# Kernel optimization log

Hardware: AMD Instinct MI355X
Metric: run time of the kernel (lower is better)

Reference implementation:

```python
import jax, jax.numpy as jnp
import numpy as np

N_NODES = 50000
N_EDGES = 800000
HIDDEN = 128
DIST_BUCKETS = 20


def setup_inputs() -> dict:
    key = jax.random.key(0)
    k = jax.random.split(key, 6)
    x = jax.random.normal(k[0], (N_NODES, HIDDEN), dtype=jnp.float32)
    edge_index = jax.random.randint(k[1], (2, N_EDGES), 0, N_NODES, dtype=jnp.int64)
    distances = jax.random.randint(k[2], (N_EDGES,), 0, 999, dtype=jnp.int64)
    W1 = jax.random.normal(k[3], (2 * HIDDEN, HIDDEN), dtype=jnp.float32) * 0.1
    W2 = jax.random.normal(k[4], (2 * HIDDEN, 1), dtype=jnp.float32) * 0.1
    dist_emb_table = jax.random.normal(k[5], (DIST_BUCKETS, HIDDEN), dtype=jnp.float32) * 0.1
    return {"x": x, "edge_index": edge_index, "distances": distances,
            "W1": W1, "W2": W2, "dist_emb_table": dist_emb_table}


def reference(x, edge_index, distances, W1, W2, dist_emb_table):
    n_nodes = x.shape[0]
    buckets = distances // 50                          # [E] in [0, 20)
    src = x[edge_index[0]]                             # [E, H]
    tgt = x[edge_index[1]]                             # [E, H]
    h = jnp.concatenate([src, tgt], axis=1) @ W1       # [E, H]
    h = jax.nn.leaky_relu(h, negative_slope=0.2)
    de = dist_emb_table[buckets]                       # [E, H]
    att = jnp.concatenate([h, de], axis=1) @ W2        # [E, 1]
    att = jnp.exp(jax.nn.sigmoid(att))                 # [E, 1]
    src_w = src * att                                  # [E, H]
    agg = jax.ops.segment_sum(src_w, edge_index[1], num_segments=n_nodes)   # [N, H]
    att_agg = jax.ops.segment_sum(att, edge_index[1], num_segments=n_nodes) # [N, 1]
    out = agg / (att_agg + 1e-6)
    return jax.nn.relu(out)
```

## Files before the change

### kernel.cpp

```cpp
#include <hip/hip_runtime.h>

#define HIDDEN 128
#define NBUCKETS 20
#define CSRCAP 64

typedef unsigned int uint32;
typedef unsigned short u16;
typedef unsigned long long u64;
typedef __attribute__((ext_vector_type(8))) short bf16x8;
typedef __attribute__((ext_vector_type(4))) float f32x4;

__device__ __forceinline__ u16 f32_to_bf16(float f) {
    uint32 u = __float_as_uint(f);
    return (u16)((u + 0x7fffu + ((u >> 16) & 1u)) >> 16);
}
__device__ __forceinline__ float bf_lo(uint32 u) { return __uint_as_float(u << 16); }
__device__ __forceinline__ float bf_hi(uint32 u) { return __uint_as_float(u & 0xffff0000u); }

__global__ void prep_kernel(const float* __restrict__ W1, u16* __restrict__ W1T,
                            int* __restrict__ cur, int n_nodes,
                            const float* __restrict__ table,
                            const float* __restrict__ W2,
                            float* __restrict__ de_dot) {
    int idx = blockIdx.x * 256 + threadIdx.x;
    int n = idx >> 7, k = idx & 127;
    int srow = (n < 128) ? k : (128 + k);
    W1T[idx] = f32_to_bf16(W1[srow * HIDDEN + (n & 127)]);
    for (int i = idx; i < n_nodes; i += 32768) cur[i] = 0;
    if (blockIdx.x < 5) {
        int w = blockIdx.x * 4 + (threadIdx.x >> 6);
        int lane = threadIdx.x & 63;
        if (w < NBUCKETS) {
            float a = fmaf(table[w * HIDDEN + lane], W2[HIDDEN + lane],
                           table[w * HIDDEN + 64 + lane] * W2[HIDDEN + 64 + lane]);
#pragma unroll
            for (int off = 32; off > 0; off >>= 1) a += __shfl_xor(a, off, 64);
            if (lane == 0) de_dot[w] = a;
        }
    }
}

__global__ __launch_bounds__(256)
void gemm_scatter_kernel(const float* __restrict__ x, const u16* __restrict__ W1T,
                         const int* __restrict__ edge_index,
                         const int* __restrict__ distances,
                         int* __restrict__ cur, uint32* __restrict__ csr_sb,
                         uint32* __restrict__ xyu, u16* __restrict__ z16,
                         int n_nodes, int n_edges) {
    __shared__ bf16x8 lds_a[16][16];
    __shared__ u16 lds_c[4][16][72];

    int tid = threadIdx.x;

    int e = blockIdx.x * 256 + tid;
    if (e < n_edges) {
        int s = edge_index[e];
        int t = edge_index[n_edges + e];
        uint32 bk = (uint32)(distances[e] / 50);
        int pos = atomicAdd(&cur[t], 1);
        csr_sb[((size_t)t << 6) + pos] = (uint32)s | (bk << 16);
    }

    int row_base = blockIdx.x * 16;
    if (row_base >= n_nodes) return;

    {
        int row = tid >> 4, c = tid & 15;
        int node = row_base + row;
        bf16x8 a = {};
        if (node < n_nodes) {
            const float4* xp = (const float4*)(x + (size_t)node * HIDDEN + c * 8);
            float4 v0 = xp[0], v1 = xp[1];
            a[0] = (short)f32_to_bf16(v0.x); a[1] = (short)f32_to_bf16(v0.y);
            a[2] = (short)f32_to_bf16(v0.z); a[3] = (short)f32_to_bf16(v0.w);
            a[4] = (short)f32_to_bf16(v1.x); a[5] = (short)f32_to_bf16(v1.y);
            a[6] = (short)f32_to_bf16(v1.z); a[7] = (short)f32_to_bf16(v1.w);
        }
        lds_a[c][row] = a;
    }
    __syncthreads();

    int wave = tid >> 6, lane = tid & 63;
    int m = lane & 15, kb = lane >> 4;

    bf16x8 afrag[4];
#pragma unroll
    for (int ks = 0; ks < 4; ++ks) afrag[ks] = lds_a[ks * 4 + kb][m];

#pragma unroll
    for (int ci = 0; ci < 4; ++ci) {
        int col = wave * 64 + ci * 16 + m;
        const u16* bp = W1T + (size_t)col * HIDDEN + kb * 8;
        f32x4 acc = {0.f, 0.f, 0.f, 0.f};
#pragma unroll
        for (int ks = 0; ks < 4; ++ks) {
            bf16x8 b = *(const bf16x8*)(bp + ks * 32);
            acc = __builtin_amdgcn_mfma_f32_16x16x32_bf16(afrag[ks], b, acc, 0, 0, 0);
        }
#pragma unroll
        for (int e2 = 0; e2 < 4; ++e2)
            lds_c[wave][kb * 4 + e2][ci * 16 + m] = f32_to_bf16(acc[e2]);
    }
    __syncthreads();

    {
        int r = lane >> 2, q = lane & 3;
        const u16* src = &lds_c[wave][r][q * 16];
        bf16x8 c0 = *(const bf16x8*)(src);
        bf16x8 c1 = *(const bf16x8*)(src + 8);
        int node = row_base + r;
        int colg = wave * 64 + q * 16;
        if (node < n_nodes) {
            if (colg < HIDDEN) {
                int ch = colg >> 3;
                bf16x8 xa = lds_a[ch][r];
                bf16x8 xb = lds_a[ch + 1][r];
                const uint32* xu0 = (const uint32*)&xa;
                const uint32* xu1 = (const uint32*)&xb;
                const uint32* yu0 = (const uint32*)&c0;
                const uint32* yu1 = (const uint32*)&c1;
                uint32 ow[16];
#pragma unroll
                for (int i = 0; i < 4; ++i) { ow[2*i]   = xu0[i]; ow[2*i+1]   = yu0[i]; }
#pragma unroll
                for (int i = 0; i < 4; ++i) { ow[8+2*i] = xu1[i]; ow[8+2*i+1] = yu1[i]; }
                uint32* dst = xyu + (size_t)node * 128 + colg;
#pragma unroll
                for (int i = 0; i < 4; ++i)
                    *(f32x4*)(dst + i * 4) = *(const f32x4*)(ow + i * 4);
            } else {
                u16* dst = z16 + (size_t)node * HIDDEN + colg - HIDDEN;
                *(bf16x8*)dst = c0;
                *(bf16x8*)(dst + 8) = c1;
            }
        }
    }
}

__global__ void aggregate_kernel(const uint32* __restrict__ xyu,
                                 const u16* __restrict__ z16,
                                 const float* __restrict__ W2,
                                 const uint32* __restrict__ csr_sb,
                                 const int* __restrict__ cur,
                                 const float* __restrict__ de_dot,
                                 float* __restrict__ out,
                                 int n_nodes) {
    __shared__ float d_lds[NBUCKETS];
    int tid = threadIdx.x;
    if (tid < NBUCKETS) d_lds[tid] = de_dot[tid];
    __syncthreads();

    int lane = tid & 63;
    int t = blockIdx.x * (blockDim.x >> 6) + (tid >> 6);
    if (t >= n_nodes) return;

    size_t base = (size_t)t << 6;
    int deg = cur[t];
    const uint2* __restrict__ xyp = (const uint2*)xyu;

    uint32 zv = ((const uint32*)z16)[(size_t)t * 64 + lane];
    float z0 = bf_lo(zv), z1 = bf_hi(zv);
    float2 wv = *(const float2*)(W2 + lane * 2);

    float acc0 = 0.f, acc1 = 0.f, attsum = 0.f;
    bool hiHalf = lane >= 32;
    bool hiQuarter = (lane & 16) != 0;

    for (int b = 0; b < deg; b += 64) {
        int nb = min(64, deg - b);
        uint32 rec_l = 0;
        float ded_l = 0.f;
        if (lane < nb) {
            rec_l = csr_sb[base + b + lane];
            ded_l = d_lds[rec_l >> 16];
        }
        int j = 0;
        for (; j + 4 <= nb; j += 4) {
            int sA = (int)(__shfl(rec_l, j, 64) & 0xFFFFu);
            int sB = (int)(__shfl(rec_l, j + 1, 64) & 0xFFFFu);
            int sC = (int)(__shfl(rec_l, j + 2, 64) & 0xFFFFu);
            int sD = (int)(__shfl(rec_l, j + 3, 64) & 0xFFFFu);
            float dA = __shfl(ded_l, j, 64);
            float dB = __shfl(ded_l, j + 1, 64);
            float dC = __shfl(ded_l, j + 2, 64);
            float dD = __shfl(ded_l, j + 3, 64);
            uint2 va = xyp[(size_t)sA * 64 + lane];
            uint2 vb = xyp[(size_t)sB * 64 + lane];
            uint2 vc = xyp[(size_t)sC * 64 + lane];
            uint2 vd = xyp[(size_t)sD * 64 + lane];
            float h;
            h = bf_lo(va.y) + z0; h = fmaxf(h, 0.2f * h); float pA = h * wv.x;
            h = bf_hi(va.y) + z1; h = fmaxf(h, 0.2f * h); pA = fmaf(h, wv.y, pA);
            h = bf_lo(vb.y) + z0; h = fmaxf(h, 0.2f * h); float pB = h * wv.x;
            h = bf_hi(vb.y) + z1; h = fmaxf(h, 0.2f * h); pB = fmaf(h, wv.y, pB);
            h = bf_lo(vc.y) + z0; h = fmaxf(h, 0.2f * h); float pC = h * wv.x;
            h = bf_hi(vc.y) + z1; h = fmaxf(h, 0.2f * h); pC = fmaf(h, wv.y, pC);
            h = bf_lo(vd.y) + z0; h = fmaxf(h, 0.2f * h); float pD = h * wv.x;
            h = bf_hi(vd.y) + z1; h = fmaxf(h, 0.2f * h); pD = fmaf(h, wv.y, pD);
            pA += __shfl_xor(pA, 32, 64);
            pB += __shfl_xor(pB, 32, 64);
            pC += __shfl_xor(pC, 32, 64);
            pD += __shfl_xor(pD, 32, 64);
            float rAB = hiHalf ? pB : pA;
            float rCD = hiHalf ? pD : pC;
            rAB += __shfl_xor(rAB, 16, 64);
            rCD += __shfl_xor(rCD, 16, 64);
            float rr = hiQuarter ? rCD : rAB;
#pragma unroll
            for (int off = 8; off > 0; off >>= 1) rr += __shfl_xor(rr, off, 64);
            float ded_e = hiQuarter ? (hiHalf ? dD : dC) : (hiHalf ? dB : dA);
            float att = __expf(1.f / (1.f + __expf(-(rr + ded_e))));
            float attA = __shfl(att, 0, 64);
            float attC = __shfl(att, 16, 64);
            float attB = __shfl(att, 32, 64);
            float attD = __shfl(att, 48, 64);
            acc0 = fmaf(attA, bf_lo(va.x), acc0);
            acc1 = fmaf(attA, bf_hi(va.x), acc1);
            acc0 = fmaf(attB, bf_lo(vb.x), acc0);
            acc1 = fmaf(attB, bf_hi(vb.x), acc1);
            acc0 = fmaf(attC, bf_lo(vc.x), acc0);
            acc1 = fmaf(attC, bf_hi(vc.x), acc1);
            acc0 = fmaf(attD, bf_lo(vd.x), acc0);
            acc1 = fmaf(attD, bf_hi(vd.x), acc1);
            attsum += (attA + attB) + (attC + attD);
        }
        for (; j < nb; ++j) {
            int sA = (int)(__shfl(rec_l, j, 64) & 0xFFFFu);
            float dA = __shfl(ded_l, j, 64);
            uint2 va = xyp[(size_t)sA * 64 + lane];
            float hA0 = bf_lo(va.y) + z0, hA1 = bf_hi(va.y) + z1;
            hA0 = fmaxf(hA0, 0.2f * hA0); hA1 = fmaxf(hA1, 0.2f * hA1);
            float pA = fmaf(hA0, wv.x, hA1 * wv.y);
#pragma unroll
            for (int off = 32; off > 0; off >>= 1) pA += __shfl_xor(pA, off, 64);
            float attA = __expf(1.f / (1.f + __expf(-(pA + dA))));
            acc0 = fmaf(attA, bf_lo(va.x), acc0);
            acc1 = fmaf(attA, bf_hi(va.x), acc1);
            attsum += attA;
        }
    }
    float inv = 1.f / (attsum + 1e-6f);
    float2 o;
    o.x = fmaxf(acc0 * inv, 0.f);
    o.y = fmaxf(acc1 * inv, 0.f);
    *(float2*)(out + (size_t)t * HIDDEN + lane * 2) = o;
}

static inline size_t align16(size_t v) { return (v + 15) & ~(size_t)15; }

extern "C" void kernel_launch(void* const* d_in, const int* in_sizes, int n_in,
                              void* d_out, int out_size, void* d_ws, size_t ws_size,
                              hipStream_t stream) {
    const float* x          = (const float*)d_in[0];
    const int*   edge_index = (const int*)d_in[1];
    const int*   distances  = (const int*)d_in[2];
    const float* W1         = (const float*)d_in[3];
    const float* W2         = (const float*)d_in[4];
    const float* table      = (const float*)d_in[5];

    int n_nodes = in_sizes[0] / HIDDEN;
    int n_edges = in_sizes[1] / 2;
    float* out = (float*)d_out;

    char* p = (char*)d_ws;
    int* cur       = (int*)p;                p += align16((size_t)n_nodes * 4);
    uint32* csr_sb = (uint32*)p;             p += align16((size_t)n_nodes * CSRCAP * 4);
    float* de_dot  = (float*)p;              p += align16(32 * 4);
    u16* W1T       = (u16*)p;                p += align16(256 * HIDDEN * 2);
    u16* z16       = (u16*)p;                p += align16((size_t)n_nodes * HIDDEN * 2);
    uint32* xyu    = (uint32*)p;

    prep_kernel<<<128, 256, 0, stream>>>(W1, W1T, cur, n_nodes, table, W2, de_dot);

    int ntiles = (n_nodes + 15) / 16;
    int eblocks = (n_edges + 255) / 256;
    int gblocks = (ntiles > eblocks) ? ntiles : eblocks;
    gemm_scatter_kernel<<<gblocks, 256, 0, stream>>>(
        x, W1T, edge_index, distances, cur, csr_sb, xyu, z16, n_nodes, n_edges);

    const int waves_per_block = 4;
    int ablocks = (n_nodes + waves_per_block - 1) / waves_per_block;
    aggregate_kernel<<<ablocks, 64 * waves_per_block, 0, stream>>>(
        xyu, z16, W2, csr_sb, cur, de_dot, out, n_nodes);
}
```

Measured before the change: 137.2 us.

## Process two edges and two GEMM row tiles per block, deferring atomics

Each block of the fused GEMM/scatter kernel now handles two edges per thread and two 16-row node tiles, halving the grid. Edge index and distance loads are issued up front, and the atomic CSR insertion is moved after the GEMM so the load latency overlaps with the matrix work. This amortizes per-block setup and W1T fragment loads across two tiles, at the cost of extra LDS, registers and an additional barrier per tile.

```diff
diff --git a/kernel.cpp b/kernel.cpp
--- a/kernel.cpp
+++ b/kernel.cpp
@@ -47,93 +47,118 @@
                          int* __restrict__ cur, uint32* __restrict__ csr_sb,
                          uint32* __restrict__ xyu, u16* __restrict__ z16,
                          int n_nodes, int n_edges) {
-    __shared__ bf16x8 lds_a[16][16];
+    __shared__ bf16x8 lds_a[2][16][16];
     __shared__ u16 lds_c[4][16][72];
 
     int tid = threadIdx.x;
 
-    int e = blockIdx.x * 256 + tid;
-    if (e < n_edges) {
-        int s = edge_index[e];
-        int t = edge_index[n_edges + e];
-        uint32 bk = (uint32)(distances[e] / 50);
-        int pos = atomicAdd(&cur[t], 1);
-        csr_sb[((size_t)t << 6) + pos] = (uint32)s | (bk << 16);
-    }
-
-    int row_base = blockIdx.x * 16;
-    if (row_base >= n_nodes) return;
-
-    {
-        int row = tid >> 4, c = tid & 15;
-        int node = row_base + row;
-        bf16x8 a = {};
-        if (node < n_nodes) {
-            const float4* xp = (const float4*)(x + (size_t)node * HIDDEN + c * 8);
-            float4 v0 = xp[0], v1 = xp[1];
-            a[0] = (short)f32_to_bf16(v0.x); a[1] = (short)f32_to_bf16(v0.y);
-            a[2] = (short)f32_to_bf16(v0.z); a[3] = (short)f32_to_bf16(v0.w);
-            a[4] = (short)f32_to_bf16(v1.x); a[5] = (short)f32_to_bf16(v1.y);
-            a[6] = (short)f32_to_bf16(v1.z); a[7] = (short)f32_to_bf16(v1.w);
-        }
-        lds_a[c][row] = a;
+    int e0 = blockIdx.x * 512 + tid;
+    int e1 = e0 + 256;
+    bool he0 = (e0 < n_edges), he1 = (e1 < n_edges);
+    int es0 = 0, et0 = 0, es1 = 0, et1 = 0;
+    uint32 bk0 = 0, bk1 = 0;
+    if (he0) {
+        es0 = edge_index[e0];
+        et0 = edge_index[n_edges + e0];
+        bk0 = (uint32)(distances[e0] / 50);
+    }
+    if (he1) {
+        es1 = edge_index[e1];
+        et1 = edge_index[n_edges + e1];
+        bk1 = (uint32)(distances[e1] / 50);
+    }
+
+    int rb0 = blockIdx.x * 32;
+
+#pragma unroll
+    for (int tt = 0; tt < 2; ++tt) {
+        int rb = rb0 + tt * 16;
+        if (rb < n_nodes) {
+            int row = tid >> 4, c = tid & 15;
+            int node = rb + row;
+            bf16x8 a = {};
+            if (node < n_nodes) {
+                const float4* xp = (const float4*)(x + (size_t)node * HIDDEN + c * 8);
+                float4 v0 = xp[0], v1 = xp[1];
+                a[0] = (short)f32_to_bf16(v0.x); a[1] = (short)f32_to_bf16(v0.y);
+                a[2] = (short)f32_to_bf16(v0.z); a[3] = (short)f32_to_bf16(v0.w);
+                a[4] = (short)f32_to_bf16(v1.x); a[5] = (short)f32_to_bf16(v1.y);
+                a[6] = (short)f32_to_bf16(v1.z); a[7] = (short)f32_to_bf16(v1.w);
+            }
+            lds_a[tt][c][row] = a;
+        }
     }
     __syncthreads();
 
     int wave = tid >> 6, lane = tid & 63;
     int m = lane & 15, kb = lane >> 4;
 
-    bf16x8 afrag[4];
-#pragma unroll
-    for (int ks = 0; ks < 4; ++ks) afrag[ks] = lds_a[ks * 4 + kb][m];
-
-#pragma unroll
-    for (int ci = 0; ci < 4; ++ci) {
-        int col = wave * 64 + ci * 16 + m;
-        const u16* bp = W1T + (size_t)col * HIDDEN + kb * 8;
-        f32x4 acc = {0.f, 0.f, 0.f, 0.f};
-#pragma unroll
-        for (int ks = 0; ks < 4; ++ks) {
-            bf16x8 b = *(const bf16x8*)(bp + ks * 32);
-            acc = __builtin_amdgcn_mfma_f32_16x16x32_bf16(afrag[ks], b, acc, 0, 0, 0);
-        }
-#pragma unroll
-        for (int e2 = 0; e2 < 4; ++e2)
-            lds_c[wave][kb * 4 + e2][ci * 16 + m] = f32_to_bf16(acc[e2]);
-    }
-    __syncthreads();
-
-    {
-        int r = lane >> 2, q = lane & 3;
-        const u16* src = &lds_c[wave][r][q * 16];
-        bf16x8 c0 = *(const bf16x8*)(src);
-        bf16x8 c1 = *(const bf16x8*)(src + 8);
-        int node = row_base + r;
-        int colg = wave * 64 + q * 16;
-        if (node < n_nodes) {
-            if (colg < HIDDEN) {
-                int ch = colg >> 3;
-                bf16x8 xa = lds_a[ch][r];
-                bf16x8 xb = lds_a[ch + 1][r];
-                const uint32* xu0 = (const uint32*)&xa;
-                const uint32* xu1 = (const uint32*)&xb;
-                const uint32* yu0 = (const uint32*)&c0;
-                const uint32* yu1 = (const uint32*)&c1;
-                uint32 ow[16];
-#pragma unroll
-                for (int i = 0; i < 4; ++i) { ow[2*i]   = xu0[i]; ow[2*i+1]   = yu0[i]; }
-#pragma unroll
-                for (int i = 0; i < 4; ++i) { ow[8+2*i] = xu1[i]; ow[8+2*i+1] = yu1[i]; }
-                uint32* dst = xyu + (size_t)node * 128 + colg;
-#pragma unroll
-                for (int i = 0; i < 4; ++i)
-                    *(f32x4*)(dst + i * 4) = *(const f32x4*)(ow + i * 4);
-            } else {
-                u16* dst = z16 + (size_t)node * HIDDEN + colg - HIDDEN;
-                *(bf16x8*)dst = c0;
-                *(bf16x8*)(dst + 8) = c1;
+#pragma unroll
+    for (int tt = 0; tt < 2; ++tt) {
+        int rb = rb0 + tt * 16;
+        bool ht = (rb < n_nodes);
+        if (ht) {
+            bf16x8 afrag[4];
+#pragma unroll
+            for (int ks = 0; ks < 4; ++ks) afrag[ks] = lds_a[tt][ks * 4 + kb][m];
+#pragma unroll
+            for (int ci = 0; ci < 4; ++ci) {
+                int col = wave * 64 + ci * 16 + m;
+                const u16* bp = W1T + (size_t)col * HIDDEN + kb * 8;
+                f32x4 acc = {0.f, 0.f, 0.f, 0.f};
+#pragma unroll
+                for (int ks = 0; ks < 4; ++ks) {
+                    bf16x8 b = *(const bf16x8*)(bp + ks * 32);
+                    acc = __builtin_amdgcn_mfma_f32_16x16x32_bf16(afrag[ks], b, acc, 0, 0, 0);
+                }
+#pragma unroll
+                for (int e2 = 0; e2 < 4; ++e2)
+                    lds_c[wave][kb * 4 + e2][ci * 16 + m] = f32_to_bf16(acc[e2]);
             }
         }
+        __syncthreads();
+        if (ht) {
+            int r = lane >> 2, q = lane & 3;
+            const u16* src = &lds_c[wave][r][q * 16];
+            bf16x8 c0 = *(const bf16x8*)(src);
+            bf16x8 c1 = *(const bf16x8*)(src + 8);
+            int node = rb + r;
+            int colg = wave * 64 + q * 16;
+            if (node < n_nodes) {
+                if (colg < HIDDEN) {
+                    int ch = colg >> 3;
+                    bf16x8 xa = lds_a[tt][ch][r];
+                    bf16x8 xb = lds_a[tt][ch + 1][r];
+                    const uint32* xu0 = (const uint32*)&xa;
+                    const uint32* xu1 = (const uint32*)&xb;
+                    const uint32* yu0 = (const uint32*)&c0;
+                    const uint32* yu1 = (const uint32*)&c1;
+                    uint32 ow[16];
+#pragma unroll
+                    for (int i = 0; i < 4; ++i) { ow[2*i]   = xu0[i]; ow[2*i+1]   = yu0[i]; }
+#pragma unroll
+                    for (int i = 0; i < 4; ++i) { ow[8+2*i] = xu1[i]; ow[8+2*i+1] = yu1[i]; }
+                    uint32* dst = xyu + (size_t)node * 128 + colg;
+#pragma unroll
+                    for (int i = 0; i < 4; ++i)
+                        *(f32x4*)(dst + i * 4) = *(const f32x4*)(ow + i * 4);
+                } else {
+                    u16* dst = z16 + (size_t)node * HIDDEN + colg - HIDDEN;
+                    *(bf16x8*)dst = c0;
+                    *(bf16x8*)(dst + 8) = c1;
+                }
+            }
+        }
+        if (tt == 0) __syncthreads();
+    }
+
+    if (he0) {
+        int pos = atomicAdd(&cur[et0], 1);
+        csr_sb[((size_t)et0 << 6) + pos] = (uint32)es0 | (bk0 << 16);
+    }
+    if (he1) {
+        int pos = atomicAdd(&cur[et1], 1);
+        csr_sb[((size_t)et1 << 6) + pos] = (uint32)es1 | (bk1 << 16);
     }
 }
 
@@ -272,9 +297,9 @@
 
     prep_kernel<<<128, 256, 0, stream>>>(W1, W1T, cur, n_nodes, table, W2, de_dot);
 
-    int ntiles = (n_nodes + 15) / 16;
-    int eblocks = (n_edges + 255) / 256;
-    int gblocks = (ntiles > eblocks) ? ntiles : eblocks;
+    int ntiles2 = (n_nodes + 31) / 32;
+    int eblocks2 = (n_edges + 511) / 512;
+    int gblocks = (ntiles2 > eblocks2) ? ntiles2 : eblocks2;
     gemm_scatter_kernel<<<gblocks, 256, 0, stream>>>(
         x, W1T, edge_index, distances, cur, csr_sb, xyu, z16, n_nodes, n_edges);
 
```

New measurement: 146.9 us. +7.1%, slower.
